# Kernel tuning notes

Hardware: AMD Instinct MI355X
Metric: run time of the kernel (lower is better)

Reference implementation:

```python
import jax, jax.numpy as jnp
import numpy as np

B, C, H, W = 2048, 256, 7, 7
EPS = 1e-6  # torch.nn.CosineSimilarity eps


def _masked_cos_loss(f1, f2, A):
    """Fused all-pairs masked cosine similarity.
    f1, f2: [B, C, H, W]; A: [H, W, H, W] binary mask.
    Replaces the original 7x7x7x7 Python loop of per-pixel CosineSimilarity calls.
    Returns per-batch loss [B]: sum_{ijkl: A==1} cos(f1[:,:,i,j], f2[:,:,k,l]) / (H*W*H*W).
    """
    n1 = jnp.linalg.norm(f1, axis=1)  # [B, H, W]
    n2 = jnp.linalg.norm(f2, axis=1)  # [B, H, W]
    dot = jnp.einsum('bcij,bckl->bijkl', f1, f2)  # [B, H, W, H, W]
    denom = jnp.maximum(n1[:, :, :, None, None] * n2[:, None, None, :, :], EPS)
    cos = dot / denom
    mask = (A == 1).astype(f1.dtype)
    return jnp.einsum('bijkl,ijkl->b', cos, mask) / (H * W * H * W)


def setup_inputs() -> dict:
    key = jax.random.key(0)
    k1, k2, k3, k4 = jax.random.split(key, 4)
    base_feature = jax.random.normal(k1, (B, C, H, W), dtype=jnp.float32)
    moment_feature = jax.random.normal(k2, (B, C, H, W), dtype=jnp.float32)
    base_A = jax.random.randint(k3, (H, W, H, W), 0, 2, dtype=jnp.int32)
    moment_A = jax.random.randint(k4, (H, W, H, W), 0, 2, dtype=jnp.int32)
    return {"base_feature": base_feature, "moment_feature": moment_feature,
            "base_A": base_A, "moment_A": moment_A}


def reference(base_feature, moment_feature, base_A, moment_A):
    # base_loss  = masked cos(base[i,j],   moment[k,l]) under base_A
    # moment_loss = masked cos(moment[i,j], base[k,l])  under moment_A
    base_loss = _masked_cos_loss(base_feature, moment_feature, base_A)
    moment_loss = _masked_cos_loss(moment_feature, base_feature, moment_A)
    return -base_loss - moment_loss  # [B]
```

## Files before the change

kernel.cpp:

```cpp
#include <hip/hip_runtime.h>
#include <math.h>


constexpr int NB  = 2048;
constexpr int NC  = 256;
constexpr int NP  = 49;
constexpr float EPS = 1e-6f;

constexpr int PW      = 40;
constexpr int MROW    = 49;
constexpr int BUFROWS = 4 * MROW;
constexpr int TOTROWS = 2 * BUFROWS + 15;

typedef short bf16x8 __attribute__((ext_vector_type(8)));
typedef float f32x4  __attribute__((ext_vector_type(4)));

__global__ __launch_bounds__(256, 2)
void pixpro_kernel(const float* __restrict__ gbase,
                   const float* __restrict__ gmom,
                   const int*   __restrict__ A1,
                   const int*   __restrict__ A2,
                   float*       __restrict__ out)
{
    __shared__ unsigned char wtb[NP * NP];
    __shared__ __align__(16) unsigned short mats[TOTROWS * PW];
    __shared__ float nbp[4][NP], nmp[4][NP];
    __shared__ float sbc[NP], smc[NP];
    __shared__ float redsum[4];

    const int tid  = threadIdx.x;
    const int wave = tid >> 6;
    const int lane = tid & 63;
    const int b    = blockIdx.x;

    for (int t = tid; t < NP * NP; t += 256) {
        int p = t / NP, q = t - p * NP;
        wtb[t] = (unsigned char)((A1[t] == 1 ? 1 : 0) + (A2[q * NP + p] == 1 ? 1 : 0));
    }

    const float* gB = gbase + (size_t)b * (NC * NP);
    const float* gM = gmom  + (size_t)b * (NC * NP);
    const bool   ld = (lane < NP);

    float nrmb = 0.f, nrmm = 0.f;

    auto LOADS = [&](int panel, float (&x)[2][8]) {
        if (!ld) return;
        const float* pB = gB + (32 * panel + 8 * wave) * NP + lane;
        const float* pM = gM + (32 * panel + 8 * wave) * NP + lane;
        #pragma unroll
        for (int j = 0; j < 8; ++j) x[0][j] = pB[j * NP];
        #pragma unroll
        for (int j = 0; j < 8; ++j) x[1][j] = pM[j * NP];
    };

    auto CVTWRITE = [&](int buf, float (&x)[2][8]) {
        if (!ld) return;
        #pragma unroll
        for (int f = 0; f < 2; ++f) {
            unsigned int hi[4], lo[4];
            float n = 0.f;
            #pragma unroll
            for (int jp = 0; jp < 4; ++jp) {
                float x0 = x[f][2 * jp], x1 = x[f][2 * jp + 1];
                unsigned int u0 = __float_as_uint(x0) & 0xFFFF0000u;
                unsigned int u1 = __float_as_uint(x1) & 0xFFFF0000u;
                hi[jp] = u1 | (u0 >> 16);
                float l0 = x0 - __uint_as_float(u0);
                float l1 = x1 - __uint_as_float(u1);
                unsigned int r;
                asm("v_cvt_pk_bf16_f32 %0, %1, %2" : "=v"(r) : "v"(l0), "v"(l1));
                lo[jp] = r;
                n = fmaf(x0, x0, fmaf(x1, x1, n));
            }
            if (f == 0) nrmb += n; else nrmm += n;
            unsigned short* mh = mats + ((size_t)buf * BUFROWS + (2 * f + 0) * MROW + lane) * PW + 8 * wave;
            unsigned short* ml = mats + ((size_t)buf * BUFROWS + (2 * f + 1) * MROW + lane) * PW + 8 * wave;
            *reinterpret_cast<uint4*>(mh) = make_uint4(hi[0], hi[1], hi[2], hi[3]);
            *reinterpret_cast<uint4*>(ml) = make_uint4(lo[0], lo[1], lo[2], lo[3]);
        }
    };

    f32x4 acc[4];
    const f32x4 zz = {0.f, 0.f, 0.f, 0.f};
    acc[0] = zz; acc[1] = zz; acc[2] = zz; acc[3] = zz;

    const int fr = lane & 15;
    const int kc = lane >> 4;

    auto COMPUTE = [&](int buf) {
        const unsigned short* mb = mats + (size_t)buf * BUFROWS * PW;
        const unsigned short* pA = mb + (16 * wave + fr) * PW + kc * 8;
        bf16x8 Ah = *(const bf16x8*)(pA);
        bf16x8 Al = *(const bf16x8*)(pA + MROW * PW);
        #pragma unroll
        for (int t = 0; t < 4; ++t) {
            const unsigned short* pBm = mb + (2 * MROW + 16 * t + fr) * PW + kc * 8;
            bf16x8 Bh = *(const bf16x8*)(pBm);
            bf16x8 Bl = *(const bf16x8*)(pBm + MROW * PW);
            acc[t] = __builtin_amdgcn_mfma_f32_16x16x32_bf16(Ah, Bh, acc[t], 0, 0, 0);
            acc[t] = __builtin_amdgcn_mfma_f32_16x16x32_bf16(Ah, Bl, acc[t], 0, 0, 0);
            acc[t] = __builtin_amdgcn_mfma_f32_16x16x32_bf16(Al, Bh, acc[t], 0, 0, 0);
        }
    };

    {
        float x0[2][8];
        LOADS(0, x0);
        CVTWRITE(0, x0);
    }
    __syncthreads();

    #pragma unroll 2
    for (int k = 0; k < 8; ++k) {
        float xn[2][8];
        if (k + 1 < 8) LOADS(k + 1, xn);
        COMPUTE(k & 1);
        if (k + 1 < 8) CVTWRITE((k & 1) ^ 1, xn);
        __syncthreads();
    }

    if (ld) { nbp[wave][lane] = nrmb; nmp[wave][lane] = nrmm; }
    __syncthreads();
    if (wave == 0 && ld) {
        sbc[lane] = nbp[0][lane] + nbp[1][lane] + nbp[2][lane] + nbp[3][lane];
        smc[lane] = nmp[0][lane] + nmp[1][lane] + nmp[2][lane] + nmp[3][lane];
    }
    __syncthreads();

    float nbr[4];
    #pragma unroll
    for (int r = 0; r < 4; ++r) {
        int row = 16 * wave + 4 * kc + r;
        nbr[r] = (row < NP) ? sqrtf(sbc[row]) : 0.f;
    }
    float sum = 0.f;
    #pragma unroll
    for (int t = 0; t < 4; ++t) {
        int col = 16 * t + fr;
        if (col < NP) {
            float nmc = sqrtf(smc[col]);
            #pragma unroll
            for (int r = 0; r < 4; ++r) {
                int row = 16 * wave + 4 * kc + r;
                if (row < NP) {
                    float w     = (float)wtb[row * NP + col];
                    float denom = fmaxf(nbr[r] * nmc, EPS);
                    sum += w * acc[t][r] / denom;
                }
            }
        }
    }
    #pragma unroll
    for (int m = 32; m; m >>= 1) sum += __shfl_xor(sum, m, 64);
    if (lane == 0) redsum[wave] = sum;
    __syncthreads();
    if (tid == 0)
        out[b] = -(redsum[0] + redsum[1] + redsum[2] + redsum[3]) * (1.0f / 2401.0f);
}

extern "C" void kernel_launch(void* const* d_in, const int* in_sizes, int n_in,
                              void* d_out, int out_size, void* d_ws, size_t ws_size,
                              hipStream_t stream)
{
    (void)in_sizes; (void)n_in; (void)d_ws; (void)ws_size; (void)out_size;
    const float* base = (const float*)d_in[0];
    const float* mom  = (const float*)d_in[1];
    const int*   A1   = (const int*)d_in[2];
    const int*   A2   = (const int*)d_in[3];
    float*       out  = (float*)d_out;

    pixpro_kernel<<<NB, 256, 0, stream>>>(base, mom, A1, A2, out);
}
```

Measured before the change: 229.2 us.

## Deepen global-load prefetch to three panels with lightweight LDS-only barriers

```diff
diff --git a/kernel.cpp b/kernel.cpp
--- a/kernel.cpp
+++ b/kernel.cpp
@@ -104,21 +104,27 @@
         }
     };
 
-    {
-        float x0[2][8];
-        LOADS(0, x0);
-        CVTWRITE(0, x0);
-    }
-    __syncthreads();
+    auto CBAR = [&]() {
+        asm volatile("s_waitcnt lgkmcnt(0)" ::: "memory");
+        __builtin_amdgcn_s_barrier();
+        __builtin_amdgcn_sched_barrier(0);
+    };
 
-    #pragma unroll 2
-    for (int k = 0; k < 8; ++k) {
-        float xn[2][8];
-        if (k + 1 < 8) LOADS(k + 1, xn);
-        COMPUTE(k & 1);
-        if (k + 1 < 8) CVTWRITE((k & 1) ^ 1, xn);
-        __syncthreads();
-    }
+    float xA[2][8], xB[2][8], xC[2][8];
+    LOADS(0, xA);
+    LOADS(1, xB);
+    LOADS(2, xC);
+    CVTWRITE(0, xA);
+    CBAR();
+
+    COMPUTE(0); LOADS(3, xA); CVTWRITE(1, xB); CBAR();
+    COMPUTE(1); LOADS(4, xB); CVTWRITE(0, xC); CBAR();
+    COMPUTE(0); LOADS(5, xC); CVTWRITE(1, xA); CBAR();
+    COMPUTE(1); LOADS(6, xA); CVTWRITE(0, xB); CBAR();
+    COMPUTE(0); LOADS(7, xB); CVTWRITE(1, xC); CBAR();
+    COMPUTE(1);               CVTWRITE(0, xA); CBAR();
+    COMPUTE(0);               CVTWRITE(1, xB); CBAR();
+    COMPUTE(1);
 
     if (ld) { nbp[wave][lane] = nrmb; nmp[wave][lane] = nrmm; }
     __syncthreads();
```

Measured after the change: 230.7 us. Within noise of the previous version (+0.7%).

## Stage fp32 panels via direct global-to-LDS loads and convert to bf16 in compute

Applied to the files above, without the earlier changes.

```diff
diff --git a/kernel.cpp b/kernel.cpp
--- a/kernel.cpp
+++ b/kernel.cpp
@@ -7,13 +7,19 @@
 constexpr int NP  = 49;
 constexpr float EPS = 1e-6f;
 
-constexpr int PW      = 40;
-constexpr int MROW    = 49;
-constexpr int BUFROWS = 4 * MROW;
-constexpr int TOTROWS = 2 * BUFROWS + 15;
+constexpr int GPW  = 260;
+constexpr int FSW  = 8 * GPW;
+constexpr int BUFW = 2 * FSW;
+constexpr int PSTR = 32 * NP;
 
 typedef short bf16x8 __attribute__((ext_vector_type(8)));
 typedef float f32x4  __attribute__((ext_vector_type(4)));
+typedef unsigned int uix4 __attribute__((ext_vector_type(4)));
+
+#define GLD(SRC, DST)                                                        \
+    __builtin_amdgcn_global_load_lds(                                        \
+        (const __attribute__((address_space(1))) unsigned int*)(SRC),        \
+        (__attribute__((address_space(3))) unsigned int*)(DST), 4, 0, 0)
 
 __global__ __launch_bounds__(256, 2)
 void pixpro_kernel(const float* __restrict__ gbase,
@@ -23,8 +29,7 @@
                    float*       __restrict__ out)
 {
     __shared__ unsigned char wtb[NP * NP];
-    __shared__ __align__(16) unsigned short mats[TOTROWS * PW];
-    __shared__ float nbp[4][NP], nmp[4][NP];
+    __shared__ __align__(16) float mats[2 * BUFW];
     __shared__ float sbc[NP], smc[NP];
     __shared__ float redsum[4];
 
@@ -40,91 +45,120 @@
 
     const float* gB = gbase + (size_t)b * (NC * NP);
     const float* gM = gmom  + (size_t)b * (NC * NP);
-    const bool   ld = (lane < NP);
-
-    float nrmb = 0.f, nrmm = 0.f;
-
-    auto LOADS = [&](int panel, float (&x)[2][8]) {
-        if (!ld) return;
-        const float* pB = gB + (32 * panel + 8 * wave) * NP + lane;
-        const float* pM = gM + (32 * panel + 8 * wave) * NP + lane;
-        #pragma unroll
-        for (int j = 0; j < 8; ++j) x[0][j] = pB[j * NP];
-        #pragma unroll
-        for (int j = 0; j < 8; ++j) x[1][j] = pM[j * NP];
-    };
-
-    auto CVTWRITE = [&](int buf, float (&x)[2][8]) {
-        if (!ld) return;
-        #pragma unroll
-        for (int f = 0; f < 2; ++f) {
-            unsigned int hi[4], lo[4];
-            float n = 0.f;
-            #pragma unroll
-            for (int jp = 0; jp < 4; ++jp) {
-                float x0 = x[f][2 * jp], x1 = x[f][2 * jp + 1];
-                unsigned int u0 = __float_as_uint(x0) & 0xFFFF0000u;
-                unsigned int u1 = __float_as_uint(x1) & 0xFFFF0000u;
-                hi[jp] = u1 | (u0 >> 16);
-                float l0 = x0 - __uint_as_float(u0);
-                float l1 = x1 - __uint_as_float(u1);
-                unsigned int r;
-                asm("v_cvt_pk_bf16_f32 %0, %1, %2" : "=v"(r) : "v"(l0), "v"(l1));
-                lo[jp] = r;
-                n = fmaf(x0, x0, fmaf(x1, x1, n));
-            }
-            if (f == 0) nrmb += n; else nrmm += n;
-            unsigned short* mh = mats + ((size_t)buf * BUFROWS + (2 * f + 0) * MROW + lane) * PW + 8 * wave;
-            unsigned short* ml = mats + ((size_t)buf * BUFROWS + (2 * f + 1) * MROW + lane) * PW + 8 * wave;
-            *reinterpret_cast<uint4*>(mh) = make_uint4(hi[0], hi[1], hi[2], hi[3]);
-            *reinterpret_cast<uint4*>(ml) = make_uint4(lo[0], lo[1], lo[2], lo[3]);
-        }
-    };
+
+    const int ch0 = 8 * wave + (lane & 3);
+    const int px0 = lane >> 2;
+    const float* srcAb = gB + ch0 * NP + px0;
+    const float* src3b = gB + ch0 * NP + 48;
+    const float* srcAm = gM + ch0 * NP + px0;
+    const float* src3m = gM + ch0 * NP + 48;
+
+    int stg_buf = 0;
+
+    auto STAGE = [&]() {
+        float* const d0 = mats + stg_buf + (2 * wave) * GPW;
+        float* const d1 = d0 + FSW;
+        #pragma unroll
+        for (int gl = 0; gl < 2; ++gl) {
+            GLD(srcAb + gl * 196 +  0, d0 + gl * GPW +   0);
+            GLD(srcAb + gl * 196 + 16, d0 + gl * GPW +  64);
+            GLD(srcAb + gl * 196 + 32, d0 + gl * GPW + 128);
+            GLD(src3b + gl * 196,      d0 + gl * GPW + 192);
+        }
+        #pragma unroll
+        for (int gl = 0; gl < 2; ++gl) {
+            GLD(srcAm + gl * 196 +  0, d1 + gl * GPW +   0);
+            GLD(srcAm + gl * 196 + 16, d1 + gl * GPW +  64);
+            GLD(srcAm + gl * 196 + 32, d1 + gl * GPW + 128);
+            GLD(src3m + gl * 196,      d1 + gl * GPW + 192);
+        }
+        srcAb += PSTR; src3b += PSTR; srcAm += PSTR; src3m += PSTR;
+        stg_buf ^= BUFW;
+    };
+
+    const int fr = lane & 15;
+    const int kc = lane >> 4;
 
     f32x4 acc[4];
     const f32x4 zz = {0.f, 0.f, 0.f, 0.f};
     acc[0] = zz; acc[1] = zz; acc[2] = zz; acc[3] = zz;
-
-    const int fr = lane & 15;
-    const int kc = lane >> 4;
-
-    auto COMPUTE = [&](int buf) {
-        const unsigned short* mb = mats + (size_t)buf * BUFROWS * PW;
-        const unsigned short* pA = mb + (16 * wave + fr) * PW + kc * 8;
-        bf16x8 Ah = *(const bf16x8*)(pA);
-        bf16x8 Al = *(const bf16x8*)(pA + MROW * PW);
+    float nb = 0.f;
+    float nm[4] = {0.f, 0.f, 0.f, 0.f};
+
+    auto CVT8 = [&](float4 L, float4 H, unsigned int (&hw)[4],
+                    unsigned int (&lw)[4], float& na) {
+        float xs[8] = {L.x, L.y, L.z, L.w, H.x, H.y, H.z, H.w};
+        #pragma unroll
+        for (int jp = 0; jp < 4; ++jp) {
+            float x0 = xs[2 * jp], x1 = xs[2 * jp + 1];
+            unsigned int u0 = __float_as_uint(x0) & 0xFFFF0000u;
+            unsigned int u1 = __float_as_uint(x1) & 0xFFFF0000u;
+            hw[jp] = u1 | (u0 >> 16);
+            float l0 = x0 - __uint_as_float(u0);
+            float l1 = x1 - __uint_as_float(u1);
+            unsigned int r;
+            asm("v_cvt_pk_bf16_f32 %0, %1, %2" : "=v"(r) : "v"(l0), "v"(l1));
+            lw[jp] = r;
+            na = fmaf(x0, x0, fmaf(x1, x1, na));
+        }
+    };
+    auto PACK = [](const unsigned int (&w)[4]) {
+        uix4 t; t[0] = w[0]; t[1] = w[1]; t[2] = w[2]; t[3] = w[3];
+        return *(const bf16x8*)&t;
+    };
+
+    auto COMPUTE = [&](int bufw) {
+        const float* pa = mats + bufw + (2 * kc) * GPW + (16 * wave + fr) * 4;
+        float4 aL = *(const float4*)(pa);
+        float4 aH = *(const float4*)(pa + GPW);
+        unsigned int ahw[4], alw[4];
+        CVT8(aL, aH, ahw, alw, nb);
+        bf16x8 Ah = PACK(ahw), Al = PACK(alw);
+        const float* pb = mats + bufw + FSW + (2 * kc) * GPW + fr * 4;
         #pragma unroll
         for (int t = 0; t < 4; ++t) {
-            const unsigned short* pBm = mb + (2 * MROW + 16 * t + fr) * PW + kc * 8;
-            bf16x8 Bh = *(const bf16x8*)(pBm);
-            bf16x8 Bl = *(const bf16x8*)(pBm + MROW * PW);
+            float4 bL = *(const float4*)(pb + t * 64);
+            float4 bH = *(const float4*)(pb + t * 64 + GPW);
+            unsigned int bhw[4], blw[4];
+            CVT8(bL, bH, bhw, blw, nm[t]);
+            bf16x8 Bh = PACK(bhw), Bl = PACK(blw);
             acc[t] = __builtin_amdgcn_mfma_f32_16x16x32_bf16(Ah, Bh, acc[t], 0, 0, 0);
             acc[t] = __builtin_amdgcn_mfma_f32_16x16x32_bf16(Ah, Bl, acc[t], 0, 0, 0);
             acc[t] = __builtin_amdgcn_mfma_f32_16x16x32_bf16(Al, Bh, acc[t], 0, 0, 0);
         }
     };
 
-    {
-        float x0[2][8];
-        LOADS(0, x0);
-        CVTWRITE(0, x0);
-    }
+    STAGE();
+    asm volatile("s_waitcnt vmcnt(0)" ::: "memory");
     __syncthreads();
 
     #pragma unroll 2
     for (int k = 0; k < 8; ++k) {
-        float xn[2][8];
-        if (k + 1 < 8) LOADS(k + 1, xn);
-        COMPUTE(k & 1);
-        if (k + 1 < 8) CVTWRITE((k & 1) ^ 1, xn);
-        __syncthreads();
-    }
-
-    if (ld) { nbp[wave][lane] = nrmb; nmp[wave][lane] = nrmm; }
-    __syncthreads();
-    if (wave == 0 && ld) {
-        sbc[lane] = nbp[0][lane] + nbp[1][lane] + nbp[2][lane] + nbp[3][lane];
-        smc[lane] = nmp[0][lane] + nmp[1][lane] + nmp[2][lane] + nmp[3][lane];
+        if (k < 7) STAGE();
+        __builtin_amdgcn_sched_barrier(0);
+        COMPUTE((k & 1) * BUFW);
+        asm volatile("s_waitcnt vmcnt(0) lgkmcnt(0)" ::: "memory");
+        __builtin_amdgcn_s_barrier();
+        __builtin_amdgcn_sched_barrier(0);
+    }
+
+    nb += __shfl_xor(nb, 16, 64);
+    nb += __shfl_xor(nb, 32, 64);
+    #pragma unroll
+    for (int t = 0; t < 4; ++t) {
+        nm[t] += __shfl_xor(nm[t], 16, 64);
+        nm[t] += __shfl_xor(nm[t], 32, 64);
+    }
+    if (lane < 16) {
+        int p = 16 * wave + lane;
+        if (p < NP) sbc[p] = nb;
+    }
+    if (wave == 0 && lane < 16) {
+        #pragma unroll
+        for (int t = 0; t < 4; ++t) {
+            int p = 16 * t + lane;
+            if (p < NP) smc[p] = nm[t];
+        }
     }
     __syncthreads();
 
```

Result: slower. 240.6 us (+5.0%).
